# Optimization experiments

Hardware: AMD Instinct MI355X
Metric: run time of the kernel (lower is better)

The kernel has to match this reference:

```python
import jax, jax.numpy as jnp
import numpy as np
import math

B, T, D, M, V = 16, 256, 256, 32, 50257
EPS = 1e-6


def setup_inputs() -> dict:
    key = jax.random.key(0)
    ks = jax.random.split(key, 24)
    s = 0.02
    inp = {
        'hidden_state': jax.random.normal(ks[0], (B, 2, D), jnp.float32),
        'output_sequence': jax.random.randint(ks[1], (B, T), 0, V),
        # embedding table for output tokens
        'emb_out': jax.random.normal(ks[2], (V, D), jnp.float32) * s,
        # decoder_attention (Wq,Wk,Wv are torch Linear weights [out,in], plus biases)
        'Wq1': jax.random.normal(ks[3], (D, D), jnp.float32) * s,
        'bq1': jnp.zeros((D,), jnp.float32),
        'Wk1': jax.random.normal(ks[4], (D, D), jnp.float32) * s,
        'bk1': jnp.zeros((D,), jnp.float32),
        'Wv1': jax.random.normal(ks[5], (D, D), jnp.float32) * s,
        'bv1': jnp.zeros((D,), jnp.float32),
        # decoder_attention_2
        'Wq2': jax.random.normal(ks[6], (D, D), jnp.float32) * s,
        'bq2': jnp.zeros((D,), jnp.float32),
        'Wk2': jax.random.normal(ks[7], (D, D), jnp.float32) * s,
        'bk2': jnp.zeros((D,), jnp.float32),
        'Wv2': jax.random.normal(ks[8], (D, D), jnp.float32) * s,
        'bv2': jnp.zeros((D,), jnp.float32),
        # decoder_mover / decoder_mover_2 weights: nn.Linear(D, M).weight -> [M, D]
        'mover1': jax.random.normal(ks[9], (M, D), jnp.float32) * s,
        'mover2': jax.random.normal(ks[10], (M, D), jnp.float32) * s,
        # norm2
        'gamma': jnp.ones((D,), jnp.float32),
        'beta': jnp.zeros((D,), jnp.float32),
        # vocab logits linear [V, D] + bias
        'Wvoc': jax.random.normal(ks[11], (V, D), jnp.float32) * s,
        'bvoc': jnp.zeros((V,), jnp.float32),
    }
    return inp


def _attn(q, kv, Wq, bq, Wk, bk, Wv, bv):
    # q: [B,1,D], kv: [B,M+1,D]
    Q = q @ Wq.T + bq
    K = kv @ Wk.T + bk
    Vv = kv @ Wv.T + bv
    s = jnp.einsum('bqd,bkd->bqk', Q, K) / jnp.sqrt(jnp.asarray(Q.shape[-1], Q.dtype))
    a = jax.nn.softmax(s, axis=-1)
    return jnp.einsum('bqk,bkd->bqd', a, Vv)


def _layernorm(x, gamma, beta):
    mu = jnp.mean(x, axis=-1, keepdims=True)
    var = jnp.mean((x - mu) ** 2, axis=-1, keepdims=True)
    return (x - mu) * jax.lax.rsqrt(var + EPS) * gamma + beta


def reference(hidden_state, output_sequence, emb_out,
              Wq1, bq1, Wk1, bk1, Wv1, bv1,
              Wq2, bq2, Wk2, bk2, Wv2, bv2,
              mover1, mover2, gamma, beta, Wvoc, bvoc):
    d = emb_out.shape[1]
    # Embeddings: lookup scaled by sqrt(d) (standard simple-transformer embedding)
    x = emb_out[output_sequence] * jnp.sqrt(jnp.asarray(d, jnp.float32))  # [B,T,D]
    z0 = hidden_state[:, 0:1, :]
    z1 = hidden_state[:, 1:2, :]
    b = z0.shape[0]
    mv1 = jnp.broadcast_to(mover1[None], (b, mover1.shape[0], d))  # static per step
    mv2 = jnp.broadcast_to(mover2[None], (b, mover2.shape[0], d))

    def step(carry, xt):
        z0, z1 = carry
        z0 = z0 + xt[:, None, :]
        g = jnp.concatenate([z0, mv1], axis=1)          # [B,M+1,D]
        dg = _attn(g[:, :1], g, Wq1, bq1, Wk1, bk1, Wv1, bv1)
        g2 = jnp.concatenate([z1, mv2], axis=1)
        dg2 = _attn(g2[:, :1], g2, Wq2, bq2, Wk2, bk2, Wv2, bv2)
        z0 = _layernorm(z0 + dg + dg2, gamma, beta)
        return (z0, z0), None

    (z0, z1), _ = jax.lax.scan(step, (z0, z1), jnp.swapaxes(x, 0, 1))
    logits = z0 @ Wvoc.T + bvoc                         # [B,1,V]
    y = jax.nn.log_softmax(logits, axis=-1)
    return jnp.concatenate([z0, z1], axis=1), y
```

## Files before the change

kernel.cpp:

```cpp
#include <hip/hip_runtime.h>

typedef unsigned int u32;
typedef unsigned short u16;

#define DD 256
#define TT 256
#define MM 32
#define NBATCH 16
#define VV 50257

#define WS_FLAG   0
#define WS_KV     16
#define WS_A      32784
#define WS_W12S   163856
#define WS_CB     180240
#define WS_E12    180752
#define WS_CST    180816
#define WS_ZFIN   180832
#define WS_SSUM   184928
#define WS_WPK    184944
#define WS_US     332400
#define WS_SYNC   369264

#if defined(__has_builtin)
#if __has_builtin(__builtin_amdgcn_fdot2)
#define HAS_FDOT2 1
#endif
#endif

typedef _Float16 half2_t __attribute__((ext_vector_type(2)));

__device__ __forceinline__ float bf2f(u16 v){ return __uint_as_float(((u32)v) << 16); }
__device__ __forceinline__ float ldf(const void* p, size_t i, int bf){
  return bf ? bf2f(((const u16*)p)[i]) : ((const float*)p)[i];
}
__device__ __forceinline__ u32 packh2(float a, float b){
  union { half2_t h; u32 u; } x;
  x.h[0] = (_Float16)a; x.h[1] = (_Float16)b;
  return x.u;
}
__device__ __forceinline__ float fdot2(u32 a, u32 b, float c){
  union { u32 u; half2_t h; } ua, ub;
  ua.u = a; ub.u = b;
#ifdef HAS_FDOT2
  return __builtin_amdgcn_fdot2(ua.h, ub.h, c, false);
#else
  return c + (float)ua.h[0]*(float)ub.h[0] + (float)ua.h[1]*(float)ub.h[1];
#endif
}

__device__ __forceinline__ u32 ldu(const u32* p){
  return __hip_atomic_load(p, __ATOMIC_RELAXED, __HIP_MEMORY_SCOPE_SYSTEM);
}
__device__ __forceinline__ void stu(u32* p, u32 v){
  __hip_atomic_store(p, v, __ATOMIC_RELAXED, __HIP_MEMORY_SCOPE_SYSTEM);
}
template<bool FAST>
__device__ __forceinline__ u32 ldx(const u32* p){
  return __hip_atomic_load(p, __ATOMIC_RELAXED,
      FAST ? __HIP_MEMORY_SCOPE_AGENT : __HIP_MEMORY_SCOPE_SYSTEM);
}
template<bool FAST>
__device__ __forceinline__ void stx(u32* p, u32 v){
  __hip_atomic_store(p, v, __ATOMIC_RELAXED,
      FAST ? __HIP_MEMORY_SCOPE_AGENT : __HIP_MEMORY_SCOPE_SYSTEM);
}
template<bool FAST>
__device__ __forceinline__ void stx_tag(float* p, float v, u32 tag){
  stx<FAST>((u32*)p, (__float_as_uint(v) & ~1u) | tag);
}

__global__ __launch_bounds__(256) void k_init(const u32* gam, u32* flag,
                                              float* Ssum, u32* sync, u32* usg){
  const int gtid = blockIdx.x*256 + threadIdx.x;
  if (blockIdx.x == 0){
    if (threadIdx.x == 0) *flag = (gam[0] == 0x3F800000u) ? 0u : 1u;
    if (threadIdx.x < 16) Ssum[threadIdx.x] = 0.f;
    for (int i = threadIdx.x; i < 512; i += 256) stu(&sync[i], 0u);
  }
  for (int i = gtid; i < NBATCH*2304; i += 8*256) stu(&usg[i], 1u);
}

__global__ __launch_bounds__(256) void k_prep1(
  const void* Wk1, const void* bk1, const void* Wv1, const void* bv1,
  const void* Wk2, const void* bk2, const void* Wv2, const void* bv2,
  const void* m1, const void* m2, float* KV, const u32* flagp)
{
  const int bf = (int)*flagp;
  int mat = blockIdx.x >> 5, j = blockIdx.x & 31, d = threadIdx.x;
  const void *W, *bias, *mv;
  if (mat == 0){ W = Wk1; bias = bk1; mv = m1; }
  else if (mat == 1){ W = Wv1; bias = bv1; mv = m1; }
  else if (mat == 2){ W = Wk2; bias = bk2; mv = m2; }
  else { W = Wv2; bias = bv2; mv = m2; }
  float acc = ldf(bias, d, bf);
  for (int e = 0; e < DD; ++e) acc += ldf(W, d*DD + e, bf) * ldf(mv, j*DD + e, bf);
  KV[mat*8192 + j*DD + d] = acc;
}

__global__ __launch_bounds__(256) void k_prep2(
  const void* Wq1, const void* Wk1, const void* bq1, const void* bk1,
  const void* Wq2, const void* Wk2, const void* bq2, const void* bk2,
  const float* KV, float* A, float* W12s, float* cb, float* e12, float* cst,
  const u32* flagp)
{
  const int bf = (int)*flagp;
  int blk = blockIdx.x, tid = threadIdx.x;
  if (blk < 512){
    int mat = blk >> 8, i = blk & 255;
    const void* Wq = mat ? Wq2 : Wq1;
    const void* Wk = mat ? Wk2 : Wk1;
    float acc = 0.f;
    for (int e = 0; e < DD; ++e) acc += ldf(Wq, e*DD + i, bf) * ldf(Wk, e*DD + tid, bf);
    A[mat*65536 + i*DD + tid] = acc;
  } else if (blk < 576){
    int idx = blk - 512, mat = idx >> 5, j = idx & 31;
    const void* Wq = mat ? Wq2 : Wq1;
    const float* K = KV + mat*16384;
    float acc = 0.f;
    for (int e = 0; e < DD; ++e) acc += ldf(Wq, e*DD + tid, bf) * K[j*DD + e];
    W12s[mat*8192 + j*DD + tid] = acc;
  } else if (blk < 578){
    int mat = blk - 576;
    const void* Wq = mat ? Wq2 : Wq1;
    const void* Wk = mat ? Wk2 : Wk1;
    const void* bq = mat ? bq2 : bq1;
    const void* bk = mat ? bk2 : bk1;
    float acc = 0.f;
    for (int e = 0; e < DD; ++e)
      acc += ldf(Wk, e*DD + tid, bf) * ldf(bq, e, bf) + ldf(Wq, e*DD + tid, bf) * ldf(bk, e, bf);
    cb[mat*DD + tid] = acc;
  } else {
    if (tid < 32){
      float acc = 0.f;
      for (int d = 0; d < DD; ++d) acc += ldf(bq1, d, bf) * KV[tid*DD + d];
      e12[tid] = acc;
    } else if (tid < 64){
      int j = tid - 32; float acc = 0.f;
      for (int d = 0; d < DD; ++d) acc += ldf(bq2, d, bf) * KV[16384 + j*DD + d];
      e12[32 + j] = acc;
    } else if (tid == 64){
      float acc = 0.f;
      for (int d = 0; d < DD; ++d) acc += ldf(bq1, d, bf) * ldf(bk1, d, bf);
      cst[0] = acc;
    } else if (tid == 65){
      float acc = 0.f;
      for (int d = 0; d < DD; ++d) acc += ldf(bq2, d, bf) * ldf(bk2, d, bf);
      cst[1] = acc;
    }
  }
}

__global__ __launch_bounds__(256) void k_pack(
  const float* __restrict__ A, const float* __restrict__ W12s,
  const float* __restrict__ cb, const void* __restrict__ Wv1,
  const void* __restrict__ Wv2, u32* __restrict__ Wpk, const u32* flagp)
{
  const int bf = (int)*flagp;
  int idx = blockIdx.x*256 + threadIdx.x;
  float v0 = 0.f, v1 = 0.f;
  if (idx < 131072){
    int p = idx >> 15;
    int r2 = idx & 32767;
    int e2g = r2 >> 10;
    int t = (r2 >> 2) & 255;
    int q = r2 & 3;
    int c = e2g*8 + q*2;
    if (p == 0){ v0 = A[t*DD + c]; v1 = A[t*DD + c + 1]; }
    else if (p == 1){ v0 = ldf(Wv1, t*DD + c, bf); v1 = ldf(Wv1, t*DD + c + 1, bf); }
    else if (p == 2){ v0 = A[65536 + t*DD + c]; v1 = A[65536 + t*DD + c + 1]; }
    else { v0 = ldf(Wv2, t*DD + c, bf); v1 = ldf(Wv2, t*DD + c + 1, bf); }
  } else {
    int rem = idx - 131072;
    int t = rem >> 7;
    int e2g = (rem >> 2) & 31;
    int q = rem & 3;
    int c = e2g*8 + q*2;
    if (t < 32){ v0 = W12s[t*DD + c]; v1 = W12s[t*DD + c + 1]; }
    else if (t < 64){ v0 = W12s[8192 + (t-32)*DD + c]; v1 = W12s[8192 + (t-32)*DD + c + 1]; }
    else if (t == 64){ v0 = cb[c]; v1 = cb[c + 1]; }
    else if (t == 65){ v0 = cb[DD + c]; v1 = cb[DD + c + 1]; }
  }
  Wpk[idx] = packh2(v0, v1);
}

template<bool FAST>
__device__ __forceinline__ void seq_loop(
    int tid, int b, int lane, int wv, int bf,
    int p, int h, int rl, int c, int l, int p4row, bool p4act, bool p4z1, int xi,
    float* us0, float* us1,
    const uint4* Wsl, const uint4* P4sl,
    const void* emb, const int* toks, float c1, float c2,
    float* z0s, float* z1s, u32* zp0, u32* zp1,
    const u32* V1q, const u32* V2q,
    float* a1s, float* a2s, float* red,
    const float* gs, const float* bs, const float* bv1s, const float* bv2s,
    const float* e1s, const float* e2s,
    float* zfin, float* out0, int g)
{
  const int hi = tid >> 1;
  const int sel = tid & 1;
  for (int t = 0; t < TT; ++t){
    float* usw = (t & 1) ? us1 : us0;
    const u32 tg = (u32)((t >> 1) & 1);
    float xnext = 0.f;
    if (t + 1 < TT) xnext = ldf(emb, (size_t)toks[t+1]*DD + tid, bf) * 16.0f;

    if (tid < 128) zp0[tid] = packh2(z0s[2*tid], z0s[2*tid+1]);
    else { int i = tid - 128; zp1[i] = packh2(z1s[2*i], z1s[2*i+1]); }
    __syncthreads();

    {
      const uint4* zz = ((const uint4*)((p < 2) ? zp0 : zp1)) + c*16;
      const uint4* wr = Wsl + c*2048 + rl;
      float a0 = 0.f, a1 = 0.f, a2 = 0.f, a3 = 0.f;
      #pragma unroll 8
      for (int kk = 0; kk < 16; ++kk){
        uint4 w = wr[kk*128];
        uint4 z = zz[kk];
        a0 = fdot2(w.x, z.x, a0);
        a1 = fdot2(w.y, z.y, a1);
        a2 = fdot2(w.z, z.z, a2);
        a3 = fdot2(w.w, z.w, a3);
      }
      float s = (a0 + a1) + (a2 + a3);
      s += __shfl_down(s, 1, 2);
      if (c == 0) stx_tag<FAST>(&usw[p*256 + h*128 + rl], s, tg);
    }
    if (p4act){
      const uint4* zq4 = (const uint4*)(p4z1 ? zp1 : zp0);
      uint4 w0 = P4sl[(tid >> 4 << 5) + l*2];
      uint4 w1 = P4sl[(tid >> 4 << 5) + l*2 + 1];
      uint4 za = zq4[l*2];
      uint4 zb = zq4[l*2 + 1];
      float a0 = fdot2(w0.x, za.x, 0.f);
      float a1 = fdot2(w0.y, za.y, 0.f);
      a0 = fdot2(w0.z, za.z, a0);
      a1 = fdot2(w0.w, za.w, a1);
      a0 = fdot2(w1.x, zb.x, a0);
      a1 = fdot2(w1.y, zb.y, a1);
      a0 = fdot2(w1.z, zb.z, a0);
      a1 = fdot2(w1.w, zb.w, a1);
      float s = a0 + a1;
      s += __shfl_down(s, 8, 16);
      s += __shfl_down(s, 4, 16);
      s += __shfl_down(s, 2, 16);
      s += __shfl_down(s, 1, 16);
      if (l == 0) stx_tag<FAST>(&usw[1024 + p4row], s, tg);
    }

    u32 b0, b1, b2, b3, bx;
    {
      const u32* up = (const u32*)usw;
      for (;;){
        b0 = ldx<FAST>(up + tid);
        b1 = ldx<FAST>(up + 256 + tid);
        b2 = ldx<FAST>(up + 512 + tid);
        b3 = ldx<FAST>(up + 768 + tid);
        bx = ldx<FAST>(up + xi);
        if ((((b0 ^ tg) | (b1 ^ tg) | (b2 ^ tg) | (b3 ^ tg) | (bx ^ tg)) & 1u) == 0u)
          break;
      }
    }
    float u0  = __uint_as_float(b0);
    float uv1 = __uint_as_float(b1);
    float u2  = __uint_as_float(b2);
    float uv2 = __uint_as_float(b3);
    float xf  = __uint_as_float(bx);

    float p1 = z0s[tid] * u0;
    float p2 = z1s[tid] * u2;
    #pragma unroll
    for (int off = 32; off; off >>= 1){
      p1 += __shfl_down(p1, off, 64);
      p2 += __shfl_down(p2, off, 64);
    }
    if (lane == 0){ red[wv] = p1; red[4 + wv] = p2; }
    __syncthreads();
    if (tid == 0) a1s[0] = (red[0]+red[1]+red[2]+red[3] + xf + c1) * 0.0625f;
    if (tid == 1) a2s[0] = (red[4]+red[5]+red[6]+red[7] + xf + c2) * 0.0625f;
    if (tid >= 64 && tid < 96)  a1s[tid - 63] = (xf + e1s[tid-64]) * 0.0625f;
    if (tid >= 96 && tid < 128) a2s[tid - 95] = (xf + e2s[tid-96]) * 0.0625f;
    __syncthreads();

    if (tid < 128){
      float* sm = (tid < 64) ? a1s : a2s;
      float v = (lane < 33) ? sm[lane] : -1e30f;
      float mx = v;
      #pragma unroll
      for (int off = 32; off; off >>= 1) mx = fmaxf(mx, __shfl_xor(mx, off, 64));
      float e = (lane < 33) ? expf(v - mx) : 0.f;
      float s = e;
      #pragma unroll
      for (int off = 32; off; off >>= 1) s += __shfl_xor(s, off, 64);
      if (lane < 33) sm[lane] = e / s;
    }
    __syncthreads();

    float hv1 = uv1 + bv1s[tid];
    float hv2 = uv2 + bv2s[tid];
    float dg = a1s[0] * hv1;
    float dh = a2s[0] * hv2;
    const uint4* v1p = (const uint4*)(V1q + hi*36);
    const uint4* v2p = (const uint4*)(V2q + hi*36);
    #pragma unroll
    for (int jj = 0; jj < 8; ++jj){
      uint4 w1 = v1p[jj];
      uint4 w2 = v2p[jj];
      union { u32 u; half2_t hh; } cv;
      cv.u = w1.x; dg += a1s[4*jj+1] * (sel ? (float)cv.hh[1] : (float)cv.hh[0]);
      cv.u = w1.y; dg += a1s[4*jj+2] * (sel ? (float)cv.hh[1] : (float)cv.hh[0]);
      cv.u = w1.z; dg += a1s[4*jj+3] * (sel ? (float)cv.hh[1] : (float)cv.hh[0]);
      cv.u = w1.w; dg += a1s[4*jj+4] * (sel ? (float)cv.hh[1] : (float)cv.hh[0]);
      cv.u = w2.x; dh += a2s[4*jj+1] * (sel ? (float)cv.hh[1] : (float)cv.hh[0]);
      cv.u = w2.y; dh += a2s[4*jj+2] * (sel ? (float)cv.hh[1] : (float)cv.hh[0]);
      cv.u = w2.z; dh += a2s[4*jj+3] * (sel ? (float)cv.hh[1] : (float)cv.hh[0]);
      cv.u = w2.w; dh += a2s[4*jj+4] * (sel ? (float)cv.hh[1] : (float)cv.hh[0]);
    }
    float y = z0s[tid] + dg + dh;
    float sy = y, syy = y * y;
    #pragma unroll
    for (int off = 32; off; off >>= 1){
      sy += __shfl_down(sy, off, 64);
      syy += __shfl_down(syy, off, 64);
    }
    if (lane == 0){ red[8 + wv] = sy; red[12 + wv] = syy; }
    __syncthreads();
    float Sy = red[8] + red[9] + red[10] + red[11];
    float Syy = red[12] + red[13] + red[14] + red[15];
    float mu = Sy * (1.f/DD);
    float var = Syy * (1.f/DD) - mu*mu;
    float zi = (y - mu) * rsqrtf(var + 1e-6f) * gs[tid] + bs[tid];
    if (t == TT - 1){
      if (g == 0){
        zfin[b*DD + tid] = zi;
        out0[b*2*DD + tid] = zi;
        out0[b*2*DD + DD + tid] = zi;
      }
    } else {
      z1s[tid] = zi;
      z0s[tid] = zi + xnext;
    }
    __syncthreads();
  }

  const u32 P = 0x7fffffffu;
  if (c == 0){
    stx<FAST>((u32*)&us0[p*256 + h*128 + rl], P);
    stx<FAST>((u32*)&us1[p*256 + h*128 + rl], P);
  }
  if (p4act && l == 0){
    stx<FAST>((u32*)&us0[1024 + p4row], P);
    stx<FAST>((u32*)&us1[1024 + p4row], P);
  }
}

__global__ __launch_bounds__(256) void k_seq(
    const void* __restrict__ hid, const int* __restrict__ seq,
    const void* __restrict__ emb,
    const u32* __restrict__ Wpk, const float* __restrict__ V1g,
    const float* __restrict__ V2g, const float* __restrict__ e1g,
    const float* __restrict__ e2g_, const float* __restrict__ cst,
    const void* __restrict__ bv1, const void* __restrict__ bv2,
    const void* __restrict__ gam, const void* __restrict__ bet,
    float* __restrict__ zfin, float* __restrict__ out0,
    const u32* __restrict__ flagp, float* __restrict__ usg,
    u32* __restrict__ syncg)
{
  __shared__ uint4 Wsl[4096];
  __shared__ uint4 P4sl[512];
  __shared__ u32 V1q[128*36], V2q[128*36];
  __shared__ float z0s[DD], z1s[DD];
  __shared__ __align__(16) u32 zp0[128], zp1[128];
  __shared__ float a1s[33], a2s[33];
  __shared__ float red[16];
  __shared__ float gs[DD], bs[DD], bv1s[DD], bv2s[DD];
  __shared__ float e1s[MM], e2s[MM];
  __shared__ int toks[TT];
  __shared__ u32 fastsh;

  const int tid = threadIdx.x;
  const int wg = blockIdx.x;
  const int b = wg & 15;
  const int g = wg >> 4;
  const int p = g >> 1;
  const int h = g & 1;
  const int rl = tid >> 1;
  const int c = tid & 1;
  const int lane = tid & 63;
  const int wv = tid >> 6;
  const int bf = (int)*flagp;

  float* us0 = usg + b*2304;
  float* us1 = us0 + 1152;
  u32* det = syncg + b*32;

  u32 myxcd = 0;
  asm volatile("s_getreg_b32 %0, hwreg(HW_REG_XCC_ID)" : "=s"(myxcd));
  if (tid == 0){
    stu(&det[g], myxcd + 1u);
    for (;;){
      u32 v0 = ldu(&det[0]), v1 = ldu(&det[1]), v2 = ldu(&det[2]), v3 = ldu(&det[3]);
      u32 v4 = ldu(&det[4]), v5 = ldu(&det[5]), v6 = ldu(&det[6]), v7 = ldu(&det[7]);
      if (v0 && v1 && v2 && v3 && v4 && v5 && v6 && v7){
        fastsh = (v0==v1 && v1==v2 && v2==v3 && v3==v4 && v4==v5 && v5==v6 && v6==v7)
                 ? 1u : 0u;
        break;
      }
    }
  }

  const uint4* Wp = (const uint4*)Wpk;
  for (int i = tid; i < 4096; i += 256){
    int kk = i >> 7, rr = i & 127;
    Wsl[kk*128 + rr] = Wp[p*8192 + kk*256 + h*128 + rr];
  }
  for (int i = tid; i < 512; i += 256){
    int rr = i >> 5, ee = i & 31;
    P4sl[rr*32 + ee] = Wp[32768 + (g*16 + rr)*32 + ee];
  }
  for (int i = tid; i < 4096; i += 256){
    int hi2 = i >> 5, j = i & 31;
    V1q[hi2*36 + j] = packh2(V1g[j*DD + 2*hi2], V1g[j*DD + 2*hi2 + 1]);
    V2q[hi2*36 + j] = packh2(V2g[j*DD + 2*hi2], V2g[j*DD + 2*hi2 + 1]);
  }
  for (int r = tid; r < TT; r += 256) toks[r] = seq[b*TT + r];
  gs[tid] = ldf(gam, tid, bf); bs[tid] = ldf(bet, tid, bf);
  bv1s[tid] = ldf(bv1, tid, bf); bv2s[tid] = ldf(bv2, tid, bf);
  if (tid < MM){ e1s[tid] = e1g[tid]; e2s[tid] = e2g_[tid]; }
  const float c1 = cst[0], c2 = cst[1];
  __syncthreads();
  z1s[tid] = ldf(hid, b*2*DD + DD + tid, bf);
  z0s[tid] = ldf(hid, b*2*DD + tid, bf) + ldf(emb, (size_t)toks[0]*DD + tid, bf) * 16.0f;
  const bool fast = (fastsh != 0);
  __syncthreads();

  const int p4row = g*16 + (tid >> 4);
  const int l = tid & 15;
  const bool p4act = (p4row < 66);
  const bool p4z1 = (p4row >= 32 && p4row < 64) || (p4row == 65);

  int xi;
  if (tid < 2) xi = 1088 + tid;
  else if (tid >= 64 && tid < 128) xi = 1024 + (tid - 64);
  else xi = tid;

  if (fast)
    seq_loop<true >(tid, b, lane, wv, bf, p, h, rl, c, l, p4row, p4act, p4z1, xi,
                    us0, us1, Wsl, P4sl, emb, toks, c1, c2, z0s, z1s, zp0, zp1,
                    V1q, V2q, a1s, a2s, red, gs, bs, bv1s, bv2s, e1s, e2s,
                    zfin, out0, g);
  else
    seq_loop<false>(tid, b, lane, wv, bf, p, h, rl, c, l, p4row, p4act, p4z1, xi,
                    us0, us1, Wsl, P4sl, emb, toks, c1, c2, z0s, z1s, zp0, zp1,
                    V1q, V2q, a1s, a2s, red, gs, bs, bv1s, bv2s, e1s, e2s,
                    zfin, out0, g);
}

__global__ __launch_bounds__(256) void k_logits(
    const float* __restrict__ zfin, const void* __restrict__ Wvoc,
    const void* __restrict__ bvoc, float* __restrict__ Ssum,
    float* __restrict__ out1, const u32* __restrict__ flagp)
{
  __shared__ float zfs[NBATCH][DD];
  const int tid = threadIdx.x;
  const int bf = (int)*flagp;
  for (int r = tid; r < NBATCH*DD; r += 256) zfs[r >> 8][r & 255] = zfin[r];
  __syncthreads();

  const int v = blockIdx.x*256 + tid;
  float acc[NBATCH];
  const bool ok = (v < VV);
  float bias = ok ? ldf(bvoc, v, bf) : 0.f;
  #pragma unroll
  for (int b = 0; b < NBATCH; ++b) acc[b] = bias;

  if (ok){
    if (bf){
      const uint4* wr = ((const uint4*)Wvoc) + (size_t)v*32;
      for (int gg = 0; gg < 32; ++gg){
        uint4 u = wr[gg];
        float w0 = __uint_as_float(u.x << 16), w1 = __uint_as_float(u.x & 0xffff0000u);
        float w2 = __uint_as_float(u.y << 16), w3 = __uint_as_float(u.y & 0xffff0000u);
        float w4 = __uint_as_float(u.z << 16), w5 = __uint_as_float(u.z & 0xffff0000u);
        float w6 = __uint_as_float(u.w << 16), w7 = __uint_as_float(u.w & 0xffff0000u);
        const int cc = gg*8;
        #pragma unroll
        for (int b = 0; b < NBATCH; ++b){
          const float* zc = &zfs[b][cc];
          acc[b] += w0*zc[0] + w1*zc[1] + w2*zc[2] + w3*zc[3]
                  + w4*zc[4] + w5*zc[5] + w6*zc[6] + w7*zc[7];
        }
      }
    } else {
      const float4* wr = ((const float4*)Wvoc) + (size_t)v*64;
      for (int gg = 0; gg < 64; ++gg){
        float4 u = wr[gg];
        const int cc = gg*4;
        #pragma unroll
        for (int b = 0; b < NBATCH; ++b){
          const float* zc = &zfs[b][cc];
          acc[b] += u.x*zc[0] + u.y*zc[1] + u.z*zc[2] + u.w*zc[3];
        }
      }
    }
    #pragma unroll
    for (int b = 0; b < NBATCH; ++b) out1[(size_t)b*VV + v] = acc[b];
  }

  #pragma unroll
  for (int b = 0; b < NBATCH; ++b){
    float pp = ok ? expf(acc[b]) : 0.f;
    #pragma unroll
    for (int off = 32; off; off >>= 1) pp += __shfl_down(pp, off, 64);
    if ((tid & 63) == 0) atomicAdd(&Ssum[b], pp);
  }
}

__global__ __launch_bounds__(256) void k_final(
    const float* __restrict__ Ssum, float* __restrict__ out1)
{
  const int v = blockIdx.x*256 + threadIdx.x;
  const int b = blockIdx.y;
  if (v < VV){
    float ls = logf(Ssum[b]);
    size_t i = (size_t)b*VV + v;
    out1[i] = out1[i] - ls;
  }
}

extern "C" void kernel_launch(void* const* d_in, const int* in_sizes, int n_in,
                              void* d_out, int out_size, void* d_ws, size_t ws_size,
                              hipStream_t stream)
{
  (void)in_sizes; (void)n_in; (void)out_size; (void)ws_size;
  const void* hid  = d_in[0];
  const int*  seq  = (const int*)d_in[1];
  const void* emb  = d_in[2];
  const void* Wq1  = d_in[3];
  const void* bq1  = d_in[4];
  const void* Wk1  = d_in[5];
  const void* bk1  = d_in[6];
  const void* Wv1  = d_in[7];
  const void* bv1  = d_in[8];
  const void* Wq2  = d_in[9];
  const void* bq2  = d_in[10];
  const void* Wk2  = d_in[11];
  const void* bk2  = d_in[12];
  const void* Wv2  = d_in[13];
  const void* bv2  = d_in[14];
  const void* m1   = d_in[15];
  const void* m2   = d_in[16];
  const void* gam  = d_in[17];
  const void* bet  = d_in[18];
  const void* Wvoc = d_in[19];
  const void* bvoc = d_in[20];

  float* wsf    = (float*)d_ws;
  u32*   flag   = (u32*)(wsf + WS_FLAG);
  float* KV     = wsf + WS_KV;
  float* A      = wsf + WS_A;
  float* W12s   = wsf + WS_W12S;
  float* cb     = wsf + WS_CB;
  float* e12    = wsf + WS_E12;
  float* cst    = wsf + WS_CST;
  float* zfin   = wsf + WS_ZFIN;
  float* Ssum   = wsf + WS_SSUM;
  u32*   Wpk    = (u32*)(wsf + WS_WPK);
  float* usg    = wsf + WS_US;
  u32*   syncg  = (u32*)(wsf + WS_SYNC);

  float* out0 = (float*)d_out;
  float* out1 = out0 + NBATCH*2*DD;

  k_init<<<8, 256, 0, stream>>>((const u32*)gam, flag, Ssum, syncg, (u32*)usg);
  k_prep1<<<128, 256, 0, stream>>>(Wk1,bk1,Wv1,bv1,Wk2,bk2,Wv2,bv2,m1,m2,KV,flag);
  k_prep2<<<579, 256, 0, stream>>>(Wq1,Wk1,bq1,bk1,Wq2,Wk2,bq2,bk2,KV,A,W12s,cb,e12,cst,flag);
  k_pack<<<576, 256, 0, stream>>>(A,W12s,cb,Wv1,Wv2,Wpk,flag);
  k_seq<<<NBATCH*8, 256, 0, stream>>>(hid, seq, emb, Wpk, KV+8192, KV+24576,
                                      e12, e12+32, cst, bv1, bv2, gam, bet, zfin, out0,
                                      flag, usg, syncg);
  k_logits<<<197, 256, 0, stream>>>(zfin, Wvoc, bvoc, Ssum, out1, flag);
  k_final<<<dim3(197, NBATCH), 256, 0, stream>>>(Ssum, out1);
}
```

Measured before the change: 1.666 ms.

## Restructure sequential step: interleaved exchange layout, register state, fdot2 attention-value mix

Reorganises the per-step inter-workgroup exchange buffer so each thread polls two 64-bit loads instead of four strided 32-bit loads. The z state moves from shared memory into registers. The softmax is folded into one pass per wave, which removes a barrier. The value mix now packs the attention weights to fp16 and uses fdot2 over a transposed VP layout. Embedding prefetch moves two steps ahead, and the trailing sentinel stores are removed. This cuts barriers and LDS traffic on the serial critical path, at the cost of extra fp16 rounding on the attention weights and a tighter register budget.

Result: no change. 1.664 ms (-0.1%).

```diff
diff --git a/kernel.cpp b/kernel.cpp
--- a/kernel.cpp
+++ b/kernel.cpp
@@ -2,6 +2,7 @@
 
 typedef unsigned int u32;
 typedef unsigned short u16;
+typedef unsigned long long u64;
 
 #define DD 256
 #define TT 256
@@ -29,6 +30,7 @@
 #endif
 
 typedef _Float16 half2_t __attribute__((ext_vector_type(2)));
+typedef __fp16 fp16x2_t __attribute__((ext_vector_type(2)));
 
 __device__ __forceinline__ float bf2f(u16 v){ return __uint_as_float(((u32)v) << 16); }
 __device__ __forceinline__ float ldf(const void* p, size_t i, int bf){
@@ -37,6 +39,11 @@
 __device__ __forceinline__ u32 packh2(float a, float b){
   union { half2_t h; u32 u; } x;
   x.h[0] = (_Float16)a; x.h[1] = (_Float16)b;
+  return x.u;
+}
+__device__ __forceinline__ u32 pkrtz(float a, float b){
+  union { fp16x2_t h; u32 u; } x;
+  x.h = __builtin_amdgcn_cvt_pkrtz(a, b);
   return x.u;
 }
 __device__ __forceinline__ float fdot2(u32 a, u32 b, float c){
@@ -56,7 +63,12 @@
   __hip_atomic_store(p, v, __ATOMIC_RELAXED, __HIP_MEMORY_SCOPE_SYSTEM);
 }
 template<bool FAST>
-__device__ __forceinline__ u32 ldx(const u32* p){
+__device__ __forceinline__ u32 ldx32(const u32* p){
+  return __hip_atomic_load(p, __ATOMIC_RELAXED,
+      FAST ? __HIP_MEMORY_SCOPE_AGENT : __HIP_MEMORY_SCOPE_SYSTEM);
+}
+template<bool FAST>
+__device__ __forceinline__ u64 ldx64(const u64* p){
   return __hip_atomic_load(p, __ATOMIC_RELAXED,
       FAST ? __HIP_MEMORY_SCOPE_AGENT : __HIP_MEMORY_SCOPE_SYSTEM);
 }
@@ -186,35 +198,44 @@
 
 template<bool FAST>
 __device__ __forceinline__ void seq_loop(
-    int tid, int b, int lane, int wv, int bf,
-    int p, int h, int rl, int c, int l, int p4row, bool p4act, bool p4z1, int xi,
+    int tid, int b, int g, int lane, int wv, int bf,
+    int p, int h, int rl, int c, int l, int p4row, bool p4act, bool p4z1,
+    int p4slot, int xi,
     float* us0, float* us1,
-    const uint4* Wsl, const uint4* P4sl,
-    const void* emb, const int* toks, float c1, float c2,
-    float* z0s, float* z1s, u32* zp0, u32* zp1,
-    const u32* V1q, const u32* V2q,
-    float* a1s, float* a2s, float* red,
+    const uint4* Wsl, const uint4* P4sl, const u32* VP1, const u32* VP2,
+    u32* zp0, u32* zp1, u32* pa1sh, u32* pa2sh,
+    float* a10sh, float* a20sh, float* red,
     const float* gs, const float* bs, const float* bv1s, const float* bv2s,
-    const float* e1s, const float* e2s,
-    float* zfin, float* out0, int g)
-{
-  const int hi = tid >> 1;
-  const int sel = tid & 1;
+    const float* e1s, const float* e2s, const int* toks, const void* emb,
+    float c1, float c2, float* zfin, float* out0,
+    float zr0, float zr1)
+{
+  float xc = ldf(emb, (size_t)toks[1]*DD + tid, bf) * 16.f;
+  float xn = ldf(emb, (size_t)toks[2]*DD + tid, bf) * 16.f;
+  const uint4* vp1 = (const uint4*)(VP1 + tid*20);
+  const uint4* vp2 = (const uint4*)(VP2 + tid*20);
+  const uint4* pp1 = (const uint4*)pa1sh;
+  const uint4* pp2 = (const uint4*)pa2sh;
+
   for (int t = 0; t < TT; ++t){
     float* usw = (t & 1) ? us1 : us0;
     const u32 tg = (u32)((t >> 1) & 1);
-    float xnext = 0.f;
-    if (t + 1 < TT) xnext = ldf(emb, (size_t)toks[t+1]*DD + tid, bf) * 16.0f;
-
-    if (tid < 128) zp0[tid] = packh2(z0s[2*tid], z0s[2*tid+1]);
-    else { int i = tid - 128; zp1[i] = packh2(z1s[2*i], z1s[2*i+1]); }
+
+    {
+      float n0 = __shfl_down(zr0, 1, 64);
+      float n1 = __shfl_down(zr1, 1, 64);
+      if (!(tid & 1)){
+        zp0[tid >> 1] = pkrtz(zr0, n0);
+        zp1[tid >> 1] = pkrtz(zr1, n1);
+      }
+    }
     __syncthreads();
 
     {
       const uint4* zz = ((const uint4*)((p < 2) ? zp0 : zp1)) + c*16;
       const uint4* wr = Wsl + c*2048 + rl;
       float a0 = 0.f, a1 = 0.f, a2 = 0.f, a3 = 0.f;
-      #pragma unroll 8
+      #pragma unroll
       for (int kk = 0; kk < 16; ++kk){
         uint4 w = wr[kk*128];
         uint4 z = zz[kk];
@@ -224,52 +245,46 @@
         a3 = fdot2(w.w, z.w, a3);
       }
       float s = (a0 + a1) + (a2 + a3);
-      s += __shfl_down(s, 1, 2);
-      if (c == 0) stx_tag<FAST>(&usw[p*256 + h*128 + rl], s, tg);
+      s += __shfl_xor(s, 1, 64);
+      if (c == 0) stx_tag<FAST>(&usw[(h*128 + rl)*4 + p], s, tg);
     }
     if (p4act){
       const uint4* zq4 = (const uint4*)(p4z1 ? zp1 : zp0);
-      uint4 w0 = P4sl[(tid >> 4 << 5) + l*2];
-      uint4 w1 = P4sl[(tid >> 4 << 5) + l*2 + 1];
-      uint4 za = zq4[l*2];
-      uint4 zb = zq4[l*2 + 1];
-      float a0 = fdot2(w0.x, za.x, 0.f);
-      float a1 = fdot2(w0.y, za.y, 0.f);
-      a0 = fdot2(w0.z, za.z, a0);
-      a1 = fdot2(w0.w, za.w, a1);
-      a0 = fdot2(w1.x, zb.x, a0);
-      a1 = fdot2(w1.y, zb.y, a1);
-      a0 = fdot2(w1.z, zb.z, a0);
-      a1 = fdot2(w1.w, zb.w, a1);
-      float s = a0 + a1;
-      s += __shfl_down(s, 8, 16);
-      s += __shfl_down(s, 4, 16);
-      s += __shfl_down(s, 2, 16);
-      s += __shfl_down(s, 1, 16);
-      if (l == 0) stx_tag<FAST>(&usw[1024 + p4row], s, tg);
-    }
-
-    u32 b0, b1, b2, b3, bx;
+      const uint4* pr = P4sl + ((tid >> 4) << 5);
+      uint4 w0 = pr[l*2], w1 = pr[l*2 + 1];
+      uint4 za = zq4[l*2], zb = zq4[l*2 + 1];
+      float a0 = fdot2(w0.x, za.x, 0.f), a1 = fdot2(w0.y, za.y, 0.f);
+      a0 = fdot2(w0.z, za.z, a0); a1 = fdot2(w0.w, za.w, a1);
+      a0 = fdot2(w1.x, zb.x, a0); a1 = fdot2(w1.y, zb.y, a1);
+      a0 = fdot2(w1.z, zb.z, a0); a1 = fdot2(w1.w, zb.w, a1);
+      float s4 = a0 + a1;
+      s4 += __shfl_down(s4, 8, 16);
+      s4 += __shfl_down(s4, 4, 16);
+      s4 += __shfl_down(s4, 2, 16);
+      s4 += __shfl_down(s4, 1, 16);
+      if (l == 0) stx_tag<FAST>(&usw[1024 + p4slot], s4, tg);
+    }
+
+    u32 q0, q1, q2, q3, x;
     {
-      const u32* up = (const u32*)usw;
+      const u64* pa = (const u64*)((const u32*)usw + tid*4);
+      const u32* pxb = (const u32*)usw + 1024 + xi;
       for (;;){
-        b0 = ldx<FAST>(up + tid);
-        b1 = ldx<FAST>(up + 256 + tid);
-        b2 = ldx<FAST>(up + 512 + tid);
-        b3 = ldx<FAST>(up + 768 + tid);
-        bx = ldx<FAST>(up + xi);
-        if ((((b0 ^ tg) | (b1 ^ tg) | (b2 ^ tg) | (b3 ^ tg) | (bx ^ tg)) & 1u) == 0u)
+        u64 a01 = ldx64<FAST>(pa);
+        u64 a23 = ldx64<FAST>(pa + 1);
+        x = ldx32<FAST>(pxb);
+        q0 = (u32)a01; q1 = (u32)(a01 >> 32);
+        q2 = (u32)a23; q3 = (u32)(a23 >> 32);
+        if ((((q0 ^ tg) | (q1 ^ tg) | (q2 ^ tg) | (q3 ^ tg) | (x ^ tg)) & 1u) == 0u)
           break;
       }
     }
-    float u0  = __uint_as_float(b0);
-    float uv1 = __uint_as_float(b1);
-    float u2  = __uint_as_float(b2);
-    float uv2 = __uint_as_float(b3);
-    float xf  = __uint_as_float(bx);
-
-    float p1 = z0s[tid] * u0;
-    float p2 = z1s[tid] * u2;
+
+    float x2 = 0.f;
+    if (t + 3 < TT) x2 = ldf(emb, (size_t)toks[t+3]*DD + tid, bf) * 16.f;
+
+    float p1 = zr0 * __uint_as_float(q0);
+    float p2 = zr1 * __uint_as_float(q2);
     #pragma unroll
     for (int off = 32; off; off >>= 1){
       p1 += __shfl_down(p1, off, 64);
@@ -277,56 +292,58 @@
     }
     if (lane == 0){ red[wv] = p1; red[4 + wv] = p2; }
     __syncthreads();
-    if (tid == 0) a1s[0] = (red[0]+red[1]+red[2]+red[3] + xf + c1) * 0.0625f;
-    if (tid == 1) a2s[0] = (red[4]+red[5]+red[6]+red[7] + xf + c2) * 0.0625f;
-    if (tid >= 64 && tid < 96)  a1s[tid - 63] = (xf + e1s[tid-64]) * 0.0625f;
-    if (tid >= 96 && tid < 128) a2s[tid - 95] = (xf + e2s[tid-96]) * 0.0625f;
-    __syncthreads();
-
-    if (tid < 128){
-      float* sm = (tid < 64) ? a1s : a2s;
-      float v = (lane < 33) ? sm[lane] : -1e30f;
+
+    const float xf = __uint_as_float(x);
+    if (wv < 2){
+      const float* ee = wv ? e2s : e1s;
+      float base;
+      if (lane == 0){
+        float rs = wv ? (red[4]+red[5]+red[6]+red[7] + c2)
+                      : (red[0]+red[1]+red[2]+red[3] + c1);
+        base = rs + xf;
+      } else {
+        base = xf + ((lane <= 32) ? ee[lane-1] : 0.f);
+      }
+      float v = (lane < 33) ? base * 0.0625f : -1e30f;
       float mx = v;
       #pragma unroll
       for (int off = 32; off; off >>= 1) mx = fmaxf(mx, __shfl_xor(mx, off, 64));
-      float e = (lane < 33) ? expf(v - mx) : 0.f;
-      float s = e;
+      float e = (lane < 33) ? __expf(v - mx) : 0.f;
+      float sden = e;
       #pragma unroll
-      for (int off = 32; off; off >>= 1) s += __shfl_xor(s, off, 64);
-      if (lane < 33) sm[lane] = e / s;
+      for (int off = 32; off; off >>= 1) sden += __shfl_xor(sden, off, 64);
+      float r = e / sden;
+      float rn = __shfl_down(r, 1, 64);
+      if (lane == 0){
+        if (wv) *a20sh = r; else *a10sh = r;
+      } else if ((lane & 1) && lane < 32){
+        (wv ? pa2sh : pa1sh)[lane >> 1] = pkrtz(r, rn);
+      }
     }
     __syncthreads();
 
-    float hv1 = uv1 + bv1s[tid];
-    float hv2 = uv2 + bv2s[tid];
-    float dg = a1s[0] * hv1;
-    float dh = a2s[0] * hv2;
-    const uint4* v1p = (const uint4*)(V1q + hi*36);
-    const uint4* v2p = (const uint4*)(V2q + hi*36);
+    float a10 = *a10sh, a20 = *a20sh;
+    float dg = a10 * (__uint_as_float(q1) + bv1s[tid]);
+    float dh = a20 * (__uint_as_float(q3) + bv2s[tid]);
     #pragma unroll
-    for (int jj = 0; jj < 8; ++jj){
-      uint4 w1 = v1p[jj];
-      uint4 w2 = v2p[jj];
-      union { u32 u; half2_t hh; } cv;
-      cv.u = w1.x; dg += a1s[4*jj+1] * (sel ? (float)cv.hh[1] : (float)cv.hh[0]);
-      cv.u = w1.y; dg += a1s[4*jj+2] * (sel ? (float)cv.hh[1] : (float)cv.hh[0]);
-      cv.u = w1.z; dg += a1s[4*jj+3] * (sel ? (float)cv.hh[1] : (float)cv.hh[0]);
-      cv.u = w1.w; dg += a1s[4*jj+4] * (sel ? (float)cv.hh[1] : (float)cv.hh[0]);
-      cv.u = w2.x; dh += a2s[4*jj+1] * (sel ? (float)cv.hh[1] : (float)cv.hh[0]);
-      cv.u = w2.y; dh += a2s[4*jj+2] * (sel ? (float)cv.hh[1] : (float)cv.hh[0]);
-      cv.u = w2.z; dh += a2s[4*jj+3] * (sel ? (float)cv.hh[1] : (float)cv.hh[0]);
-      cv.u = w2.w; dh += a2s[4*jj+4] * (sel ? (float)cv.hh[1] : (float)cv.hh[0]);
-    }
-    float y = z0s[tid] + dg + dh;
+    for (int q4 = 0; q4 < 4; ++q4){
+      uint4 w1 = vp1[q4], w2 = vp2[q4];
+      uint4 A1v = pp1[q4], A2v = pp2[q4];
+      dg = fdot2(A1v.x, w1.x, dg); dg = fdot2(A1v.y, w1.y, dg);
+      dg = fdot2(A1v.z, w1.z, dg); dg = fdot2(A1v.w, w1.w, dg);
+      dh = fdot2(A2v.x, w2.x, dh); dh = fdot2(A2v.y, w2.y, dh);
+      dh = fdot2(A2v.z, w2.z, dh); dh = fdot2(A2v.w, w2.w, dh);
+    }
+    float y = zr0 + dg + dh;
     float sy = y, syy = y * y;
     #pragma unroll
     for (int off = 32; off; off >>= 1){
-      sy += __shfl_down(sy, off, 64);
+      sy  += __shfl_down(sy, off, 64);
       syy += __shfl_down(syy, off, 64);
     }
     if (lane == 0){ red[8 + wv] = sy; red[12 + wv] = syy; }
     __syncthreads();
-    float Sy = red[8] + red[9] + red[10] + red[11];
+    float Sy  = red[8] + red[9] + red[10] + red[11];
     float Syy = red[12] + red[13] + red[14] + red[15];
     float mu = Sy * (1.f/DD);
     float var = Syy * (1.f/DD) - mu*mu;
@@ -338,24 +355,14 @@
         out0[b*2*DD + DD + tid] = zi;
       }
     } else {
-      z1s[tid] = zi;
-      z0s[tid] = zi + xnext;
-    }
-    __syncthreads();
-  }
-
-  const u32 P = 0x7fffffffu;
-  if (c == 0){
-    stx<FAST>((u32*)&us0[p*256 + h*128 + rl], P);
-    stx<FAST>((u32*)&us1[p*256 + h*128 + rl], P);
-  }
-  if (p4act && l == 0){
-    stx<FAST>((u32*)&us0[1024 + p4row], P);
-    stx<FAST>((u32*)&us1[1024 + p4row], P);
-  }
-}
-
-__global__ __launch_bounds__(256) void k_seq(
+      zr1 = zi;
+      zr0 = zi + xc;
+    }
+    xc = xn; xn = x2;
+  }
+}
+
+__global__ __launch_bounds__(256, 1) void k_seq(
     const void* __restrict__ hid, const int* __restrict__ seq,
     const void* __restrict__ emb,
     const u32* __restrict__ Wpk, const float* __restrict__ V1g,
@@ -369,10 +376,11 @@
 {
   __shared__ uint4 Wsl[4096];
   __shared__ uint4 P4sl[512];
-  __shared__ u32 V1q[128*36], V2q[128*36];
-  __shared__ float z0s[DD], z1s[DD];
+  __shared__ __align__(16) u32 VP1[256*20];
+  __shared__ __align__(16) u32 VP2[256*20];
   __shared__ __align__(16) u32 zp0[128], zp1[128];
-  __shared__ float a1s[33], a2s[33];
+  __shared__ __align__(16) u32 pa1sh[16], pa2sh[16];
+  __shared__ float a10sh, a20sh;
   __shared__ float red[16];
   __shared__ float gs[DD], bs[DD], bv1s[DD], bv2s[DD];
   __shared__ float e1s[MM], e2s[MM];
@@ -420,9 +428,9 @@
     P4sl[rr*32 + ee] = Wp[32768 + (g*16 + rr)*32 + ee];
   }
   for (int i = tid; i < 4096; i += 256){
-    int hi2 = i >> 5, j = i & 31;
-    V1q[hi2*36 + j] = packh2(V1g[j*DD + 2*hi2], V1g[j*DD + 2*hi2 + 1]);
-    V2q[hi2*36 + j] = packh2(V2g[j*DD + 2*hi2], V2g[j*DD + 2*hi2 + 1]);
+    int d = i >> 4, jj = i & 15;
+    VP1[d*20 + jj] = packh2(V1g[(2*jj)*DD + d], V1g[(2*jj+1)*DD + d]);
+    VP2[d*20 + jj] = packh2(V2g[(2*jj)*DD + d], V2g[(2*jj+1)*DD + d]);
   }
   for (int r = tid; r < TT; r += 256) toks[r] = seq[b*TT + r];
   gs[tid] = ldf(gam, tid, bf); bs[tid] = ldf(bet, tid, bf);
@@ -430,8 +438,8 @@
   if (tid < MM){ e1s[tid] = e1g[tid]; e2s[tid] = e2g_[tid]; }
   const float c1 = cst[0], c2 = cst[1];
   __syncthreads();
-  z1s[tid] = ldf(hid, b*2*DD + DD + tid, bf);
-  z0s[tid] = ldf(hid, b*2*DD + tid, bf) + ldf(emb, (size_t)toks[0]*DD + tid, bf) * 16.0f;
+  float zr1 = ldf(hid, b*2*DD + DD + tid, bf);
+  float zr0 = ldf(hid, b*2*DD + tid, bf) + ldf(emb, (size_t)toks[0]*DD + tid, bf) * 16.0f;
   const bool fast = (fastsh != 0);
   __syncthreads();
 
@@ -439,22 +447,21 @@
   const int l = tid & 15;
   const bool p4act = (p4row < 66);
   const bool p4z1 = (p4row >= 32 && p4row < 64) || (p4row == 65);
-
-  int xi;
-  if (tid < 2) xi = 1088 + tid;
-  else if (tid >= 64 && tid < 128) xi = 1024 + (tid - 64);
-  else xi = tid;
+  const int p4slot = (p4row < 32) ? (1 + p4row)
+                   : (p4row < 64) ? (3 + p4row)
+                   : (p4row == 64) ? 0 : 34;
+  const int xi = ((wv & 1) ? 34 : 0) + ((lane <= 32) ? lane : 0);
 
   if (fast)
-    seq_loop<true >(tid, b, lane, wv, bf, p, h, rl, c, l, p4row, p4act, p4z1, xi,
-                    us0, us1, Wsl, P4sl, emb, toks, c1, c2, z0s, z1s, zp0, zp1,
-                    V1q, V2q, a1s, a2s, red, gs, bs, bv1s, bv2s, e1s, e2s,
-                    zfin, out0, g);
+    seq_loop<true >(tid, b, g, lane, wv, bf, p, h, rl, c, l, p4row, p4act, p4z1,
+                    p4slot, xi, us0, us1, Wsl, P4sl, VP1, VP2, zp0, zp1,
+                    pa1sh, pa2sh, &a10sh, &a20sh, red, gs, bs, bv1s, bv2s,
+                    e1s, e2s, toks, emb, c1, c2, zfin, out0, zr0, zr1);
   else
-    seq_loop<false>(tid, b, lane, wv, bf, p, h, rl, c, l, p4row, p4act, p4z1, xi,
-                    us0, us1, Wsl, P4sl, emb, toks, c1, c2, z0s, z1s, zp0, zp1,
-                    V1q, V2q, a1s, a2s, red, gs, bs, bv1s, bv2s, e1s, e2s,
-                    zfin, out0, g);
+    seq_loop<false>(tid, b, g, lane, wv, bf, p, h, rl, c, l, p4row, p4act, p4z1,
+                    p4slot, xi, us0, us1, Wsl, P4sl, VP1, VP2, zp0, zp1,
+                    pa1sh, pa2sh, &a10sh, &a20sh, red, gs, bs, bv1s, bv2s,
+                    e1s, e2s, toks, emb, c1, c2, zfin, out0, zr0, zr1);
 }
 
 __global__ __launch_bounds__(256) void k_logits(
```
